# Optimization experiments

Measured on AMD Instinct MI355X. Metric: run time of the kernel, lower is better.

The kernel has to match this reference:

```python
import jax, jax.numpy as jnp
import numpy as np

B, P, M, W = 32, 4096, 12, 9
IN_C, OUT_C = 64, 64
IN_PN_PAD = P + 1  # in_point_num + 1 padding row


def setup_inputs() -> dict:
    key = jax.random.key(0)
    k1, k2, k3, k4 = jax.random.split(key, 4)
    in_pc_pad = jax.random.normal(k1, (B, IN_PN_PAD, IN_C), dtype=jnp.float32)
    weights = jax.random.normal(k2, (W, OUT_C * IN_C), dtype=jnp.float32)
    bias = jnp.zeros((OUT_C,), dtype=jnp.float32)
    w_weights = jax.random.normal(k3, (P, M, W), dtype=jnp.float32) / (9.0 * W)
    neighbor_id_lstlst = jax.random.randint(k4, (P, M), 0, IN_PN_PAD, dtype=jnp.int64)
    neighbor_mask_lst = jnp.ones((P, M), dtype=jnp.float32)
    return {
        "in_pc_pad": in_pc_pad,
        "weights": weights,
        "bias": bias,
        "w_weights": w_weights,
        "neighbor_id_lstlst": neighbor_id_lstlst,
        "neighbor_mask_lst": neighbor_mask_lst,
    }


def reference(in_pc_pad, weights, bias, w_weights, neighbor_id_lstlst, neighbor_mask_lst):
    # gather neighbor features: [B, P, M, IN_C]
    in_neighbors = in_pc_pad[:, neighbor_id_lstlst]
    # mask the per-(point,neighbor) basis coefficients: [P, M, W]
    w2 = w_weights * neighbor_mask_lst[:, :, None]
    # synthesize per-(point,neighbor) weight matrices from basis: [P, M, OUT_C, IN_C]
    wmat = jnp.einsum('pmw,wc->pmc', w2, weights).reshape(P, M, OUT_C, IN_C)
    # batched matvec + neighbor-sum reduce (fused over m): [B, P, OUT_C]
    out_pc = jnp.einsum('pmoi,bpmi->bpo', wmat, in_neighbors)
    return out_pc + bias
```

## Files before the change

### kernel.cpp

```cpp
#include <hip/hip_runtime.h>
#include <hip/hip_bf16.h>

#define NB 32
#define NP 4096
#define NM 12
#define NW 9
#define NC 64
#define PN_PAD 4097
#define KDIM (NW * NC)
#define KSTEPS (KDIM / 32)
#define AROW 584

#define WSW_BYTES (KDIM * NC * 2)
#define W2_OFFSET WSW_BYTES

typedef __attribute__((ext_vector_type(8))) short short8;
typedef __attribute__((ext_vector_type(4))) float float4v;

__device__ __forceinline__ unsigned short f32_to_bf16(float f) {
    union { float f; unsigned u; } v; v.f = f;
    unsigned r = v.u + 0x7FFFu + ((v.u >> 16) & 1u);
    return (unsigned short)(r >> 16);
}

__device__ __forceinline__ uint2 pack_bf16x4(float4v v) {
    union { float f; unsigned u; } a0, a1, a2, a3;
    a0.f = v[0]; a1.f = v[1]; a2.f = v[2]; a3.f = v[3];
    unsigned u0 = a0.u + 0x8000u, u1 = a1.u + 0x8000u;
    unsigned u2 = a2.u + 0x8000u, u3 = a3.u + 0x8000u;
    uint2 r;
    r.x = __builtin_amdgcn_perm(u1, u0, 0x07060302u);
    r.y = __builtin_amdgcn_perm(u3, u2, 0x07060302u);
    return r;
}

__global__ void prep(const float* __restrict__ w,
                     const float* __restrict__ ww,
                     const float* __restrict__ mask,
                     unsigned short* __restrict__ wsw,
                     float* __restrict__ w2d) {
    int idx = blockIdx.x * 256 + threadIdx.x;
    if (idx < KDIM * NC) {
        int j    = idx & 7;
        int lane = (idx >> 3) & 63;
        int nt   = (idx >> 9) & 3;
        int ks   = idx >> 11;
        int k = ks * 32 + ((lane >> 4) * 8) + j;
        int n = nt * 16 + (lane & 15);
        int wi = k >> 6;
        int ii = k & 63;
        wsw[idx] = f32_to_bf16(w[wi * (NC * NC) + n * NC + ii]);
    }
    if (idx < NP * NM * NW) {
        int wq = idx % NW;
        int pm = idx / NW;
        w2d[pm * 12 + wq] = ww[idx] * mask[pm];
    }
}

__global__ __launch_bounds__(512)
__attribute__((amdgpu_waves_per_eu(4, 4)))
void conv_main(const float* __restrict__ x,
               const unsigned short* __restrict__ wsw,
               const float* __restrict__ bias,
               const float* __restrict__ w2d,
               const int* __restrict__ nid,
               float* __restrict__ out)
{
    __shared__ __align__(16) unsigned short A[NB * AROW];

    const int p = blockIdx.x;
    const int tid = threadIdx.x;

    {
        const int i4 = tid & 15;
        const int b  = tid >> 4;
        const float4v* x4 = (const float4v*)x;
        const float* w2p = w2d + p * (NM * 12);
        const int* nidp = nid + p * NM;

        int nm[NM];
        #pragma unroll
        for (int m = 0; m < NM; ++m) nm[m] = nidp[m];

        float4v xv[NM];
        #pragma unroll
        for (int m = 0; m < NM; ++m)
            xv[m] = x4[(b * PN_PAD + nm[m]) * 16 + i4];

        float4v acc[NW];
        #pragma unroll
        for (int w = 0; w < NW; ++w) acc[w] = (float4v){0.f, 0.f, 0.f, 0.f};

        #pragma unroll
        for (int m = 0; m < NM; ++m) {
            #pragma unroll
            for (int w = 0; w < NW; ++w)
                acc[w] += w2p[m * 12 + w] * xv[m];
        }

        #pragma unroll
        for (int w = 0; w < NW; ++w)
            *(uint2*)&A[b * AROW + w * 64 + i4 * 4] = pack_bf16x4(acc[w]);
    }
    __syncthreads();

    {
        const int lane = tid & 63;
        const int wid  = tid >> 6;
        const int nt   = wid & 3;
        const int mt   = wid >> 2;
        const int quad = lane >> 4;
        const int l15  = lane & 15;

        float4v acc = {0.f, 0.f, 0.f, 0.f};
        const short8* Bfrags = (const short8*)wsw;
        const int arow = mt * 16 + l15;

        #pragma unroll
        for (int ks = 0; ks < KSTEPS; ++ks) {
            short8 bfrag = Bfrags[(ks * 4 + nt) * 64 + lane];
            const short8 a = *(const short8*)&A[arow * AROW + ks * 32 + quad * 8];
            acc = __builtin_amdgcn_mfma_f32_16x16x32_bf16(a, bfrag, acc, 0, 0, 0);
        }

        const int o = nt * 16 + l15;
        const float bv = bias[o];
        #pragma unroll
        for (int reg = 0; reg < 4; ++reg) {
            const int b = mt * 16 + quad * 4 + reg;
            out[(b * NP + p) * NC + o] = acc[reg] + bv;
        }
    }
}

extern "C" void kernel_launch(void* const* d_in, const int* in_sizes, int n_in,
                              void* d_out, int out_size, void* d_ws, size_t ws_size,
                              hipStream_t stream) {
    const float* x    = (const float*)d_in[0];
    const float* w    = (const float*)d_in[1];
    const float* bias = (const float*)d_in[2];
    const float* ww   = (const float*)d_in[3];
    const int*   nid  = (const int*)d_in[4];
    const float* mask = (const float*)d_in[5];
    float* out = (float*)d_out;
    unsigned short* wsw = (unsigned short*)d_ws;
    float* w2d = (float*)((char*)d_ws + W2_OFFSET);

    const int prep_elems = NP * NM * NW;
    hipLaunchKernelGGL(prep, dim3((prep_elems + 255) / 256), dim3(256), 0, stream,
                       w, ww, mask, wsw, w2d);
    hipLaunchKernelGGL(conv_main, dim3(NP), dim3(512), 0, stream,
                       x, wsw, bias, w2d, nid, out);
}
```

Before: 146.2 us.

## Stage neighbor gathers through LDS with direct global-to-LDS loads in chunks

Replaces the per-thread register gather of all 12 neighbor rows with four rounds of global_load_lds (16-byte direct-to-LDS loads), each staging 3 neighbors for all 32 batches into shared memory before the basis accumulation. This lowers register pressure from holding 12 float4 loads at once, and the waves_per_eu(4,4) attribute is dropped. The cost is extra barriers per round and serialized load/compute phases, since there is no double buffering, which may reduce memory-level parallelism compared with issuing all 12 gathers at once.

```diff
diff --git a/kernel.cpp b/kernel.cpp
--- a/kernel.cpp
+++ b/kernel.cpp
@@ -16,6 +16,10 @@
 
 typedef __attribute__((ext_vector_type(8))) short short8;
 typedef __attribute__((ext_vector_type(4))) float float4v;
+
+#define GLD_LDS16(g, l) __builtin_amdgcn_global_load_lds( \
+    (const __attribute__((address_space(1))) unsigned int*)(g), \
+    (__attribute__((address_space(3))) unsigned int*)(l), 16, 0, 0)
 
 __device__ __forceinline__ unsigned short f32_to_bf16(float f) {
     union { float f; unsigned u; } v; v.f = f;
@@ -59,7 +63,6 @@
 }
 
 __global__ __launch_bounds__(512)
-__attribute__((amdgpu_waves_per_eu(4, 4)))
 void conv_main(const float* __restrict__ x,
                const unsigned short* __restrict__ wsw,
                const float* __restrict__ bias,
@@ -67,53 +70,67 @@
                const int* __restrict__ nid,
                float* __restrict__ out)
 {
-    __shared__ __align__(16) unsigned short A[NB * AROW];
+    __shared__ __align__(16) unsigned char BUF[NB * AROW * 2];
 
     const int p = blockIdx.x;
     const int tid = threadIdx.x;
+    const int lane = tid & 63;
+    const int wid  = tid >> 6;
 
-    {
-        const int i4 = tid & 15;
-        const int b  = tid >> 4;
-        const float4v* x4 = (const float4v*)x;
-        const float* w2p = w2d + p * (NM * 12);
-        const int* nidp = nid + p * NM;
+    const float* w2p = w2d + p * (NM * 12);
+    const int* nidp = nid + p * NM;
 
-        int nm[NM];
+    int nm[NM];
+    #pragma unroll
+    for (int m = 0; m < NM; ++m) nm[m] = nidp[m];
+
+    const int b  = tid >> 4;
+    const int i4 = tid & 15;
+
+    float4v acc[NW];
+    #pragma unroll
+    for (int w = 0; w < NW; ++w) acc[w] = (float4v){0.f, 0.f, 0.f, 0.f};
+
+    #pragma unroll
+    for (int Q = 0; Q < 4; ++Q) {
         #pragma unroll
-        for (int m = 0; m < NM; ++m) nm[m] = nidp[m];
-
-        float4v xv[NM];
-        #pragma unroll
-        for (int m = 0; m < NM; ++m)
-            xv[m] = x4[(b * PN_PAD + nm[m]) * 16 + i4];
-
-        float4v acc[NW];
-        #pragma unroll
-        for (int w = 0; w < NW; ++w) acc[w] = (float4v){0.f, 0.f, 0.f, 0.f};
+        for (int j = 0; j < 3; ++j) {
+            const int I  = wid + 8 * j;
+            const int ml = I >> 3;
+            const int q  = I & 7;
+            const int m  = Q * 3 + ml;
+            const int brow = q * 4 + (lane >> 4);
+            const float* gsrc = x + ((size_t)(brow * PN_PAD + nm[m])) * 64
+                                  + (lane & 15) * 4;
+            unsigned char* ldst = BUF + (ml * 32 + q * 4) * 256;
+            GLD_LDS16(gsrc, ldst);
+        }
+        __syncthreads();
 
         #pragma unroll
-        for (int m = 0; m < NM; ++m) {
+        for (int ml = 0; ml < 3; ++ml) {
+            const float4v xv = *(const float4v*)(BUF + (ml * 32 + b) * 256 + i4 * 16);
+            const int m = Q * 3 + ml;
             #pragma unroll
             for (int w = 0; w < NW; ++w)
-                acc[w] += w2p[m * 12 + w] * xv[m];
+                acc[w] += w2p[m * 12 + w] * xv;
         }
+        __syncthreads();
+    }
 
-        #pragma unroll
-        for (int w = 0; w < NW; ++w)
-            *(uint2*)&A[b * AROW + w * 64 + i4 * 4] = pack_bf16x4(acc[w]);
-    }
+    unsigned short* A = (unsigned short*)BUF;
+    #pragma unroll
+    for (int w = 0; w < NW; ++w)
+        *(uint2*)&A[b * AROW + w * 64 + i4 * 4] = pack_bf16x4(acc[w]);
     __syncthreads();
 
     {
-        const int lane = tid & 63;
-        const int wid  = tid >> 6;
         const int nt   = wid & 3;
         const int mt   = wid >> 2;
         const int quad = lane >> 4;
         const int l15  = lane & 15;
 
-        float4v acc = {0.f, 0.f, 0.f, 0.f};
+        float4v cacc = {0.f, 0.f, 0.f, 0.f};
         const short8* Bfrags = (const short8*)wsw;
         const int arow = mt * 16 + l15;
 
@@ -121,15 +138,15 @@
         for (int ks = 0; ks < KSTEPS; ++ks) {
             short8 bfrag = Bfrags[(ks * 4 + nt) * 64 + lane];
             const short8 a = *(const short8*)&A[arow * AROW + ks * 32 + quad * 8];
-            acc = __builtin_amdgcn_mfma_f32_16x16x32_bf16(a, bfrag, acc, 0, 0, 0);
+            cacc = __builtin_amdgcn_mfma_f32_16x16x32_bf16(a, bfrag, cacc, 0, 0, 0);
         }
 
         const int o = nt * 16 + l15;
         const float bv = bias[o];
         #pragma unroll
         for (int reg = 0; reg < 4; ++reg) {
-            const int b = mt * 16 + quad * 4 + reg;
-            out[(b * NP + p) * NC + o] = acc[reg] + bv;
+            const int bb = mt * 16 + quad * 4 + reg;
+            out[(bb * NP + p) * NC + o] = cacc[reg] + bv;
         }
     }
 }
```

Measured after the change: 145.5 us. About the same (-0.5%).
